# Performance work log

Hardware: AMD Instinct MI355X
Metric: run time of the kernel (lower is better)

Reference implementation:

```python
import jax, jax.numpy as jnp
import numpy as np


def _expand_chunk(x):
    # prepend the previous bucket along the chunk axis: [b, nb, bl, ...] -> [b, nb, 2*bl, ...]
    return jnp.concatenate([jnp.roll(x, 1, axis=1), x], axis=2)


def _gather_seq(origin, idx):
    # origin [b, s, d], idx [b, s, r] -> out[b, s, :, r] = origin[b, idx[b, s, r], :]
    b = origin.shape[0]
    g = origin[jnp.arange(b)[:, None, None], idx]  # [b, s, r, d]
    return jnp.transpose(g, (0, 1, 3, 2))          # [b, s, d, r]


def _count_dup_keys(inp, rounds):
    # inp [b, s, K] int32: count duplicate key indices within a window of `rounds` in sorted order
    sort_idx = jnp.argsort(inp, axis=2)
    sorted_k = jnp.take_along_axis(inp, sort_idx, axis=2)
    unsort = jnp.argsort(sort_idx, axis=2)
    cnt = jnp.ones(inp.shape, jnp.float32)
    for i in range(1, rounds):
        eq = (sorted_k[..., i:] == sorted_k[..., :-i]).astype(jnp.float32)
        pad = jnp.zeros(inp.shape[:-1] + (i,), jnp.float32)
        cnt = cnt + jnp.concatenate([pad, eq], axis=-1) + jnp.concatenate([eq, pad], axis=-1)
    return jnp.take_along_axis(cnt, unsort, axis=2)


def setup_inputs() -> dict:
    key = jax.random.key(0)
    k1, k2, k3 = jax.random.split(key, 3)
    B_M_H, SEQ, D_K, N_ROUNDS, N_BUCKETS = 32, 2048, 64, 4, 32
    query = jax.random.normal(k1, (B_M_H, SEQ, D_K), jnp.float32)
    value = jax.random.normal(k2, (B_M_H, SEQ, D_K), jnp.float32)
    rand_matrix = jax.random.normal(k3, (B_M_H, D_K, N_ROUNDS, N_BUCKETS // 2), jnp.float32)
    return {"query": query, "value": value, "rand_matrix": rand_matrix}


def reference(query, value, rand_matrix):
    b, s, d = query.shape
    nr = rand_matrix.shape[2]
    n_buckets = 2 * rand_matrix.shape[3]
    bl = s // n_buckets  # bucket_len

    # --- LSH hashing: argmax over [proj, -proj], then make hashes unique per position ---
    proj = jnp.einsum('bsd,bdrk->bsrk', query, rand_matrix)
    hashes = jnp.argmax(jnp.concatenate([proj, -proj], axis=-1), axis=-1).astype(jnp.int32)
    hashes = hashes * s + jnp.arange(s, dtype=jnp.int32)[None, :, None]  # [b, s, nr]

    sort_idx = jnp.argsort(hashes, axis=1)      # [b, s, nr]
    unsort_idx = jnp.argsort(sort_idx, axis=1)  # [b, s, nr]

    # --- sort queries into buckets ---
    q = _gather_seq(query, sort_idx).reshape(b, n_buckets, bl, d, nr)
    k = _expand_chunk(q)  # [b, nb, 2*bl, d, nr]
    k = k * jax.lax.rsqrt(jnp.maximum(jnp.sum(k * k, axis=-2, keepdims=True), 1e-12))

    qk = jnp.einsum('bnidr,bnjdr->bnijr', q, k) / np.float32(np.sqrt(d))  # [b, nb, bl, 2bl, nr]

    # --- causal / self masks on original positions ---
    qi = sort_idx.reshape(b, n_buckets, bl, nr) % s
    ki = _expand_chunk(qi)  # [b, nb, 2bl, nr]
    mask1 = (qi[:, :, :, None, :] < ki[:, :, None, :, :]).astype(jnp.float32)
    mask2 = (qi[:, :, :, None, :] == ki[:, :, None, :, :]).astype(jnp.float32)
    qk = qk * (1 - mask1) + mask1 * (-1e9)
    qk = qk * (1 - mask2) + mask2 * (-1e5)

    # --- duplicate-key counting across rounds ---
    ki_b = jnp.broadcast_to(ki[:, :, None, :, :], (b, n_buckets, bl, 2 * bl, nr)).reshape(b, s, 2 * bl * nr)
    count_keys = _count_dup_keys(ki_b, nr).reshape(b, s, 2 * bl, nr)

    qk = qk.reshape(b, s, 2 * bl, nr)
    lse = jax.scipy.special.logsumexp(qk, axis=2)  # [b, s, nr]
    sm = jnp.exp(qk - lse[:, :, None, :]) / count_keys

    v = _gather_seq(value, sort_idx).reshape(b, n_buckets, bl, d, nr)
    vk = _expand_chunk(v)  # [b, nb, 2bl, d, nr]
    sm = sm.reshape(b, n_buckets, bl, 2 * bl, nr)
    att = jnp.einsum('bnijr,bnjdr->bnidr', sm, vk).reshape(b, s, d, nr)

    # --- unsort back to original order, per round ---
    att = jnp.transpose(att, (0, 1, 3, 2))  # [b, s, nr, d]
    att = jnp.take_along_axis(att, jnp.broadcast_to(unsort_idx[:, :, :, None], att.shape), axis=1)
    lse = jnp.take_along_axis(lse, unsort_idx, axis=1)

    # --- combine rounds weighted by softmax of logsumexp ---
    w = jax.nn.softmax(lse, axis=-1)  # [b, s, nr]
    return jnp.einsum('bsrd,bsr->bsd', att, w)
```

## Files before the change

### kernel.cpp

```cpp
#include <hip/hip_runtime.h>

typedef unsigned short u16;
typedef unsigned int   u32;
typedef short bf16x8 __attribute__((ext_vector_type(8)));
typedef float f32x16 __attribute__((ext_vector_type(16)));

#define S_  2048
#define D_  64
#define NR_ 4
#define NB_ 32

#define AS 72
#define VS 136
#define PS 136

__device__ __forceinline__ float bf2f(u16 u){ return __uint_as_float(((u32)u)<<16); }
__device__ __forceinline__ u16 f2bf(float f){
  u32 u = __float_as_uint(f);
  u32 r = (u + 0x7fffu + ((u>>16)&1u)) >> 16;
  return (u16)r;
}
__device__ __forceinline__ u32 pk2bf(float a, float b){
#if __has_builtin(__builtin_amdgcn_cvt_pk_bf16_f32)
  auto r = __builtin_amdgcn_cvt_pk_bf16_f32(a, b);
  u32 u; __builtin_memcpy(&u, &r, 4); return u;
#else
  return (u32)f2bf(a) | ((u32)f2bf(b) << 16);
#endif
}
__device__ __forceinline__ u16 f2bf1(float a){ return (u16)pk2bf(a, a); }
__device__ __forceinline__ void unpack2(u32 w, float &a, float &b){
  a = __uint_as_float(w<<16);
  b = __uint_as_float(w & 0xffff0000u);
}
__device__ __forceinline__ bf16x8 ld8(const u16* p){
  union { uint4 u; bf16x8 v; } x;
  x.u = *(const uint4*)p;
  return x.v;
}

__global__ __launch_bounds__(256, 2) void k_hash(const float* __restrict__ q,
                                                 const float* __restrict__ v,
                                                 const float* __restrict__ R,
                                                 int* __restrict__ hout,
                                                 u16* __restrict__ qb,
                                                 u16* __restrict__ vbuf,
                                                 float* __restrict__ scq){
  __shared__ float Rl[4096];
  int b   = blockIdx.x >> 3;
  int pos = (blockIdx.x & 7) * 256 + threadIdx.x;

  {
    const float4* Rg = (const float4*)(R + (size_t)b * 4096);
    float4* Rs = (float4*)Rl;
    #pragma unroll
    for (int k = 0; k < 4; k++) Rs[k*256 + threadIdx.x] = Rg[k*256 + threadIdx.x];
  }
  __syncthreads();

  const float4* q4 = (const float4*)(q + ((size_t)b * S_ + pos) * D_);
  const float4* v4 = (const float4*)(v + ((size_t)b * S_ + pos) * D_);
  uint2* qw = (uint2*)(qb   + ((size_t)b * S_ + pos) * D_);
  uint2* vw = (uint2*)(vbuf + ((size_t)b * S_ + pos) * D_);

  float acc[64];
  #pragma unroll
  for (int i = 0; i < 64; i++) acc[i] = 0.f;
  float ss = 0.f;

  #pragma unroll 4
  for (int c = 0; c < 16; c++){
    float4 wa = q4[c];
    float4 xa = v4[c];
    ss += wa.x*wa.x + wa.y*wa.y + wa.z*wa.z + wa.w*wa.w;
    qw[c] = make_uint2(pk2bf(wa.x, wa.y), pk2bf(wa.z, wa.w));
    vw[c] = make_uint2(pk2bf(xa.x, xa.y), pk2bf(xa.z, xa.w));
    float qa[4] = {wa.x, wa.y, wa.z, wa.w};
    #pragma unroll
    for (int dd = 0; dd < 4; dd++){
      int d = c * 4 + dd;
      const float4* Rr = (const float4*)(&Rl[d * 64]);
      #pragma unroll
      for (int k4 = 0; k4 < 16; k4++){
        float4 rv = Rr[k4];
        acc[k4*4+0] += qa[dd] * rv.x;
        acc[k4*4+1] += qa[dd] * rv.y;
        acc[k4*4+2] += qa[dd] * rv.z;
        acc[k4*4+3] += qa[dd] * rv.w;
      }
    }
  }
  scq[(size_t)b * S_ + pos] = rsqrtf(fmaxf(ss, 1e-12f)) * 0.125f;

  #pragma unroll
  for (int r = 0; r < 4; r++){
    float bv = acc[r*16]; int bi = 0;
    #pragma unroll
    for (int m = 1; m < 32; m++){
      float vv = (m < 16) ? acc[r*16 + m] : -acc[r*16 + m - 16];
      if (vv > bv){ bv = vv; bi = m; }
    }
    hout[((size_t)b * NR_ + r) * S_ + pos] = bi;
  }
}

__global__ __launch_bounds__(256) void k_sort(const int* __restrict__ h,
                                              int* __restrict__ sidx,
                                              int* __restrict__ chk){
  __shared__ int cnt[32][257];
  __shared__ int base[32];
  int br = blockIdx.x;
  const int* hb = h + (size_t)br * S_;
  int t = threadIdx.x;

  #pragma unroll
  for (int hh = 0; hh < 32; hh++) cnt[hh][t] = 0;
  __syncthreads();

  int hv[8];
  const int4* hb4 = (const int4*)hb;
  int4 a0 = hb4[t*2], a1 = hb4[t*2+1];
  hv[0]=a0.x; hv[1]=a0.y; hv[2]=a0.z; hv[3]=a0.w;
  hv[4]=a1.x; hv[5]=a1.y; hv[6]=a1.z; hv[7]=a1.w;
  #pragma unroll
  for (int k = 0; k < 8; k++) cnt[hv[k]][t]++;
  __syncthreads();

  int wave = t >> 6, lane = t & 63;
  for (int hh = wave*8; hh < wave*8 + 8; hh++){
    int vals[4]; int s0 = 0;
    #pragma unroll
    for (int k = 0; k < 4; k++){ vals[k] = cnt[hh][lane*4+k]; s0 += vals[k]; }
    int incl = s0;
    #pragma unroll
    for (int off = 1; off < 64; off <<= 1){
      int o = __shfl_up(incl, off, 64);
      if (lane >= off) incl += o;
    }
    int run = incl - s0;
    #pragma unroll
    for (int k = 0; k < 4; k++){ int tmp = vals[k]; cnt[hh][lane*4+k] = run; run += tmp; }
    if (lane == 63) base[hh] = incl;
  }
  __syncthreads();
  if (t == 0){
    int run = 0;
    #pragma unroll
    for (int hh = 0; hh < 32; hh++){ int tot = base[hh]; base[hh] = run; run += tot; }
  }
  __syncthreads();

  int p0 = t * 8;
  #pragma unroll
  for (int k = 0; k < 8; k++){
    int hh = hv[k];
    int c = cnt[hh][t];
    int slot = base[hh] + c;
    cnt[hh][t] = c + 1;
    sidx[(size_t)br * S_ + slot]    = p0 + k;
    chk [(size_t)br * S_ + p0 + k]  = slot >> 6;
  }
}

__global__ __launch_bounds__(256, 4) void k_attn(const u16* __restrict__ qb,
                                                 const u16* __restrict__ vb,
                                                 const int* __restrict__ sidx,
                                                 const int* __restrict__ chk,
                                                 const float* __restrict__ scq,
                                                 float* __restrict__ lse_ws,
                                                 u16*  __restrict__ att_ws){
  __shared__ u16 A[128*AS];
  __shared__ u16 SM[64*PS];
  __shared__ int   pkey[128];
  __shared__ float rcnt[128];
  __shared__ float sc[128];

  int blk = blockIdx.x;
  int b = blk >> 7, r = (blk >> 5) & 3, n = blk & 31;
  int npv = (n + 31) & 31;
  int t = threadIdx.x;
  int lane = t & 63, w = t >> 6;
  int la = lane & 31, hh = lane >> 5;
  int coff = hh * 8;
  const int* sb = sidx + ((size_t)b * NR_ + r) * S_;

  if (t < 128){
    int p = (t < 64) ? sb[npv*64 + t] : sb[n*64 + (t - 64)];
    pkey[t] = p;
    int c = 0;
    #pragma unroll
    for (int rr = 0; rr < 4; rr++){
      int ch = chk[((size_t)b * NR_ + rr) * S_ + p];
      c += (ch == n) || (ch == npv);
    }
    if (c < 1) c = 1;
    rcnt[t] = 1.0f / (float)c;
    sc[t] = scq[(size_t)b * S_ + p];
  }
  __syncthreads();

  {
    int row = t >> 1, half = t & 1;
    const uint4* src = (const uint4*)(qb + ((size_t)b*S_ + pkey[row])*D_) + half*4;
    uint4* dst = (uint4*)(&A[row*AS + half*32]);
    #pragma unroll
    for (int k = 0; k < 4; k++) dst[k] = src[k];
  }
  int jp = t & 63, dgrp = t >> 6;
  uint4 va0, va1, vb0, vb1;
  {
    const uint4* s0 = (const uint4*)(vb + ((size_t)b*S_ + pkey[2*jp  ])*D_ + dgrp*16);
    const uint4* s1 = (const uint4*)(vb + ((size_t)b*S_ + pkey[2*jp+1])*D_ + dgrp*16);
    va0 = s0[0]; va1 = s0[1]; vb0 = s1[0]; vb1 = s1[1];
  }
  __syncthreads();

  {
    int jt = w;
    f32x16 acc0, acc1;
    #pragma unroll
    for (int i = 0; i < 16; i++){ acc0[i] = 0.f; acc1[i] = 0.f; }
    int arow  = (jt*32 + la) * AS;
    int brow0 = (64 + la) * AS;
    int brow1 = (96 + la) * AS;
    #pragma unroll
    for (int ks = 0; ks < 4; ks++){
      int o = ks*16 + coff;
      bf16x8 af = ld8(&A[arow  + o]);
      bf16x8 b0 = ld8(&A[brow0 + o]);
      bf16x8 b1 = ld8(&A[brow1 + o]);
      acc0 = __builtin_amdgcn_mfma_f32_32x32x16_bf16(af, b0, acc0, 0, 0, 0);
      acc1 = __builtin_amdgcn_mfma_f32_32x32x16_bf16(af, b1, acc1, 0, 0, 0);
    }
    int pj[16]; float scj[16];
    #pragma unroll
    for (int g = 0; g < 4; g++){
      int j0 = jt*32 + g*8 + 4*hh;
      #pragma unroll
      for (int m = 0; m < 4; m++){ pj[g*4+m] = pkey[j0+m]; scj[g*4+m] = sc[j0+m]; }
    }
    #pragma unroll
    for (int e = 0; e < 2; e++){
      int i = e*32 + la;
      int pi = pkey[64 + i];
      #pragma unroll
      for (int g = 0; g < 4; g++){
        float l[4];
        #pragma unroll
        for (int m = 0; m < 4; m++){
          int reg = g*4 + m;
          float x = (e ? acc1[reg] : acc0[reg]) * scj[reg];
          if (pi < pj[reg])       x = -1000000000.0f;
          else if (pi == pj[reg]) x = -100000.0f;
          l[m] = x;
        }
        int j0 = jt*32 + g*8 + 4*hh;
        *(uint2*)(&SM[i*PS + j0]) = make_uint2(pk2bf(l[0], l[1]), pk2bf(l[2], l[3]));
      }
    }
  }
  __syncthreads();

  {
    int srow = t >> 2, seg = t & 3;
    uint4 u[4];
    const uint4* p4 = (const uint4*)(&SM[srow*PS + seg*32]);
    #pragma unroll
    for (int k = 0; k < 4; k++) u[k] = p4[k];
    float vals[32];
    #pragma unroll
    for (int k = 0; k < 4; k++){
      unpack2(u[k].x, vals[k*8+0], vals[k*8+1]);
      unpack2(u[k].y, vals[k*8+2], vals[k*8+3]);
      unpack2(u[k].z, vals[k*8+4], vals[k*8+5]);
      unpack2(u[k].w, vals[k*8+6], vals[k*8+7]);
    }
    float mx = -3.0e38f;
    #pragma unroll
    for (int k = 0; k < 32; k++) mx = fmaxf(mx, vals[k]);
    float sl = 0.f;
    #pragma unroll
    for (int k = 0; k < 32; k++){ vals[k] = __expf(vals[k] - mx); sl += vals[k]; }
    float mxg = fmaxf(mx, __shfl_xor(mx, 1, 64));
    mxg = fmaxf(mxg, __shfl_xor(mxg, 2, 64));
    float scale = __expf(mx - mxg);
    float s = sl * scale;
    s += __shfl_xor(s, 1, 64);
    s += __shfl_xor(s, 2, 64);
    float f = scale / s;
    const float4* rc4 = (const float4*)(&rcnt[seg*32]);
    u32 ob[16];
    #pragma unroll
    for (int k4 = 0; k4 < 8; k4++){
      float4 rc = rc4[k4];
      ob[k4*2+0] = pk2bf(vals[k4*4+0]*f*rc.x, vals[k4*4+1]*f*rc.y);
      ob[k4*2+1] = pk2bf(vals[k4*4+2]*f*rc.z, vals[k4*4+3]*f*rc.w);
    }
    uint4* d4 = (uint4*)(&SM[srow*PS + seg*32]);
    #pragma unroll
    for (int k = 0; k < 4; k++)
      d4[k] = make_uint4(ob[4*k], ob[4*k+1], ob[4*k+2], ob[4*k+3]);
    if (seg == 0)
      lse_ws[((size_t)b*S_ + pkey[64 + srow])*NR_ + r] = mxg + __logf(s);
  }

  {
    u32 au[8] = {va0.x, va0.y, va0.z, va0.w, va1.x, va1.y, va1.z, va1.w};
    u32 bu[8] = {vb0.x, vb0.y, vb0.z, vb0.w, vb1.x, vb1.y, vb1.z, vb1.w};
    u32* vtp = (u32*)A;
    #pragma unroll
    for (int k = 0; k < 8; k++){
      int d0 = dgrp*16 + 2*k;
      u32 even = (au[k] & 0xffffu) | (bu[k] << 16);
      u32 odd  = (au[k] >> 16)     | (bu[k] & 0xffff0000u);
      vtp[ d0      * (VS/2) + jp] = even;
      vtp[(d0 + 1) * (VS/2) + jp] = odd;
    }
  }
  __syncthreads();

  {
    int Mt2 = w >> 1, Nt2 = w & 1;
    f32x16 acc;
    #pragma unroll
    for (int i = 0; i < 16; i++) acc[i] = 0.f;
    int arow = (Mt2*32 + la) * VS;
    int brow = (Nt2*32 + la) * PS;
    #pragma unroll
    for (int ks = 0; ks < 8; ks++){
      int o = ks*16 + coff;
      bf16x8 af = ld8(&A[arow + o]);
      bf16x8 bf = ld8(&SM[brow + o]);
      acc = __builtin_amdgcn_mfma_f32_32x32x16_bf16(af, bf, acc, 0, 0, 0);
    }
    int i = Nt2*32 + la;
    int p = pkey[64 + i];
    u16* base = att_ws + (((size_t)b*S_ + p)*NR_ + r)*D_ + Mt2*32 + 4*hh;
    #pragma unroll
    for (int g = 0; g < 4; g++){
      uint2 val = make_uint2(pk2bf(acc[4*g+0], acc[4*g+1]),
                             pk2bf(acc[4*g+2], acc[4*g+3]));
      *(uint2*)(base + g*8) = val;
    }
  }
}

__global__ __launch_bounds__(256) void k_comb(const float* __restrict__ lse_ws,
                                              const u16* __restrict__ att_ws,
                                              float* __restrict__ out){
  size_t idx4 = (size_t)blockIdx.x * 256 + threadIdx.x;
  size_t pd = idx4 >> 4;
  int d0 = (int)(idx4 & 15) * 4;
  float4 lv = *(const float4*)(lse_ws + pd * 4);
  float m = fmaxf(fmaxf(lv.x, lv.y), fmaxf(lv.z, lv.w));
  float e0 = __expf(lv.x - m), e1 = __expf(lv.y - m);
  float e2 = __expf(lv.z - m), e3 = __expf(lv.w - m);
  float inv = 1.0f / (e0 + e1 + e2 + e3);
  e0 *= inv; e1 *= inv; e2 *= inv; e3 *= inv;
  const u16* a = att_ws + pd * 256 + d0;
  uint2 u0 = *(const uint2*)(a);
  uint2 u1 = *(const uint2*)(a + 64);
  uint2 u2 = *(const uint2*)(a + 128);
  uint2 u3 = *(const uint2*)(a + 192);
  float4 o;
  float a0,b0,a1,b1,a2,b2,a3,b3;
  unpack2(u0.x,a0,b0); unpack2(u1.x,a1,b1); unpack2(u2.x,a2,b2); unpack2(u3.x,a3,b3);
  o.x = a0*e0 + a1*e1 + a2*e2 + a3*e3;
  o.y = b0*e0 + b1*e1 + b2*e2 + b3*e3;
  unpack2(u0.y,a0,b0); unpack2(u1.y,a1,b1); unpack2(u2.y,a2,b2); unpack2(u3.y,a3,b3);
  o.z = a0*e0 + a1*e1 + a2*e2 + a3*e3;
  o.w = b0*e0 + b1*e1 + b2*e2 + b3*e3;
  *(float4*)(out + pd * D_ + d0) = o;
}

extern "C" void kernel_launch(void* const* d_in, const int* in_sizes, int n_in,
                              void* d_out, int out_size, void* d_ws, size_t ws_size,
                              hipStream_t stream){
  const float* q = (const float*)d_in[0];
  const float* v = (const float*)d_in[1];
  const float* R = (const float*)d_in[2];

  char* w = (char*)d_ws;
  int*   h    = (int*)  (w + 0);
  int*   sidx = (int*)  (w + (size_t)(1u << 20));
  int*   chkA = (int*)  (w + (size_t)(2u << 20));
  float* lse  = (float*)(w + (size_t)(3u << 20));
  u16*   att  = (u16*)  (w + (size_t)(4u << 20));
  u16*   qb   = (u16*)  (w + (size_t)(36u << 20));
  u16*   vbuf = (u16*)  (w + (size_t)(44u << 20));
  float* scq  = (float*)(w + (size_t)(52u << 20));
  float* out  = (float*)d_out;

  k_hash <<<256,  256, 0, stream>>>(q, v, R, h, qb, vbuf, scq);
  k_sort <<<128,  256, 0, stream>>>(h, sidx, chkA);
  k_attn <<<4096, 256, 0, stream>>>(qb, vbuf, sidx, chkA, scq, lse, att);
  k_comb <<<4096, 256, 0, stream>>>(lse, att, out);
}
```

Before: 150.7 us.

## Compute softmax in MFMA registers with cross-wave partial max/sum reduction

Softmax over the QK logits now runs directly on the MFMA accumulator registers. Each wave computes per-row partial max and sum, combines the two half-waves with shuffles, and exchanges partials across waves through small shared arrays. This removes the bf16 round trip of raw logits through shared memory and the separate re-read pass, and keeps logits in fp32 until the final probabilities are written. In exchange it holds more live registers, so the occupancy hint in launch bounds drops from 4 to 3 blocks.

```diff
diff --git a/kernel.cpp b/kernel.cpp
--- a/kernel.cpp
+++ b/kernel.cpp
@@ -162,7 +162,7 @@
   }
 }
 
-__global__ __launch_bounds__(256, 4) void k_attn(const u16* __restrict__ qb,
+__global__ __launch_bounds__(256, 3) void k_attn(const u16* __restrict__ qb,
                                                  const u16* __restrict__ vb,
                                                  const int* __restrict__ sidx,
                                                  const int* __restrict__ chk,
@@ -174,6 +174,8 @@
   __shared__ int   pkey[128];
   __shared__ float rcnt[128];
   __shared__ float sc[128];
+  __shared__ float pm[4*64];
+  __shared__ float ps[4*64];
 
   int blk = blockIdx.x;
   int b = blk >> 7, r = (blk >> 5) & 3, n = blk & 31;
@@ -215,6 +217,8 @@
   }
   __syncthreads();
 
+  float e0[16], e1[16];
+  float ml0, ml1;
   {
     int jt = w;
     f32x16 acc0, acc1;
@@ -239,71 +243,70 @@
       #pragma unroll
       for (int m = 0; m < 4; m++){ pj[g*4+m] = pkey[j0+m]; scj[g*4+m] = sc[j0+m]; }
     }
-    #pragma unroll
-    for (int e = 0; e < 2; e++){
-      int i = e*32 + la;
-      int pi = pkey[64 + i];
-      #pragma unroll
-      for (int g = 0; g < 4; g++){
-        float l[4];
-        #pragma unroll
-        for (int m = 0; m < 4; m++){
-          int reg = g*4 + m;
-          float x = (e ? acc1[reg] : acc0[reg]) * scj[reg];
-          if (pi < pj[reg])       x = -1000000000.0f;
-          else if (pi == pj[reg]) x = -100000.0f;
-          l[m] = x;
-        }
-        int j0 = jt*32 + g*8 + 4*hh;
-        *(uint2*)(&SM[i*PS + j0]) = make_uint2(pk2bf(l[0], l[1]), pk2bf(l[2], l[3]));
-      }
-    }
-  }
-  __syncthreads();
-
-  {
-    int srow = t >> 2, seg = t & 3;
-    uint4 u[4];
-    const uint4* p4 = (const uint4*)(&SM[srow*PS + seg*32]);
-    #pragma unroll
-    for (int k = 0; k < 4; k++) u[k] = p4[k];
-    float vals[32];
+    int pi0 = pkey[64 + la], pi1 = pkey[96 + la];
+    float x0[16], x1[16];
+    #pragma unroll
+    for (int reg = 0; reg < 16; reg++){
+      float a0v = acc0[reg] * scj[reg];
+      float a1v = acc1[reg] * scj[reg];
+      if (pi0 < pj[reg]) a0v = -1000000000.0f; else if (pi0 == pj[reg]) a0v = -100000.0f;
+      if (pi1 < pj[reg]) a1v = -1000000000.0f; else if (pi1 == pj[reg]) a1v = -100000.0f;
+      x0[reg] = a0v; x1[reg] = a1v;
+    }
+    ml0 = x0[0]; ml1 = x1[0];
+    #pragma unroll
+    for (int reg = 1; reg < 16; reg++){ ml0 = fmaxf(ml0, x0[reg]); ml1 = fmaxf(ml1, x1[reg]); }
+    float s0 = 0.f, s1 = 0.f;
+    #pragma unroll
+    for (int reg = 0; reg < 16; reg++){
+      e0[reg] = __expf(x0[reg] - ml0); s0 += e0[reg];
+      e1[reg] = __expf(x1[reg] - ml1); s1 += e1[reg];
+    }
+    float om0 = __shfl_xor(ml0, 32, 64), os0 = __shfl_xor(s0, 32, 64);
+    float om1 = __shfl_xor(ml1, 32, 64), os1 = __shfl_xor(s1, 32, 64);
+    float m20 = fmaxf(ml0, om0);
+    float m21 = fmaxf(ml1, om1);
+    float s20 = s0 * __expf(ml0 - m20) + os0 * __expf(om0 - m20);
+    float s21 = s1 * __expf(ml1 - m21) + os1 * __expf(om1 - m21);
+    if (hh == 0){
+      pm[jt*64 + la]      = m20;  ps[jt*64 + la]      = s20;
+      pm[jt*64 + 32 + la] = m21;  ps[jt*64 + 32 + la] = s21;
+    }
+  }
+  __syncthreads();
+
+  {
+    int jt = w;
+    float mg0 = pm[la],      mg1 = pm[32 + la];
+    #pragma unroll
+    for (int k = 1; k < 4; k++){
+      mg0 = fmaxf(mg0, pm[k*64 + la]);
+      mg1 = fmaxf(mg1, pm[k*64 + 32 + la]);
+    }
+    float sg0 = 0.f, sg1 = 0.f;
     #pragma unroll
     for (int k = 0; k < 4; k++){
-      unpack2(u[k].x, vals[k*8+0], vals[k*8+1]);
-      unpack2(u[k].y, vals[k*8+2], vals[k*8+3]);
-      unpack2(u[k].z, vals[k*8+4], vals[k*8+5]);
-      unpack2(u[k].w, vals[k*8+6], vals[k*8+7]);
-    }
-    float mx = -3.0e38f;
-    #pragma unroll
-    for (int k = 0; k < 32; k++) mx = fmaxf(mx, vals[k]);
-    float sl = 0.f;
-    #pragma unroll
-    for (int k = 0; k < 32; k++){ vals[k] = __expf(vals[k] - mx); sl += vals[k]; }
-    float mxg = fmaxf(mx, __shfl_xor(mx, 1, 64));
-    mxg = fmaxf(mxg, __shfl_xor(mxg, 2, 64));
-    float scale = __expf(mx - mxg);
-    float s = sl * scale;
-    s += __shfl_xor(s, 1, 64);
-    s += __shfl_xor(s, 2, 64);
-    float f = scale / s;
-    const float4* rc4 = (const float4*)(&rcnt[seg*32]);
-    u32 ob[16];
-    #pragma unroll
-    for (int k4 = 0; k4 < 8; k4++){
-      float4 rc = rc4[k4];
-      ob[k4*2+0] = pk2bf(vals[k4*4+0]*f*rc.x, vals[k4*4+1]*f*rc.y);
-      ob[k4*2+1] = pk2bf(vals[k4*4+2]*f*rc.z, vals[k4*4+3]*f*rc.w);
-    }
-    uint4* d4 = (uint4*)(&SM[srow*PS + seg*32]);
-    #pragma unroll
-    for (int k = 0; k < 4; k++)
-      d4[k] = make_uint4(ob[4*k], ob[4*k+1], ob[4*k+2], ob[4*k+3]);
-    if (seg == 0)
-      lse_ws[((size_t)b*S_ + pkey[64 + srow])*NR_ + r] = mxg + __logf(s);
-  }
-
+      sg0 += ps[k*64 + la]      * __expf(pm[k*64 + la]      - mg0);
+      sg1 += ps[k*64 + 32 + la] * __expf(pm[k*64 + 32 + la] - mg1);
+    }
+    float f0 = __expf(ml0 - mg0) / sg0;
+    float f1 = __expf(ml1 - mg1) / sg1;
+    #pragma unroll
+    for (int g = 0; g < 4; g++){
+      int j0 = jt*32 + g*8 + 4*hh;
+      float4 rc = *(const float4*)(&rcnt[j0]);
+      float p00 = e0[g*4+0]*f0*rc.x, p01 = e0[g*4+1]*f0*rc.y;
+      float p02 = e0[g*4+2]*f0*rc.z, p03 = e0[g*4+3]*f0*rc.w;
+      float p10 = e1[g*4+0]*f1*rc.x, p11 = e1[g*4+1]*f1*rc.y;
+      float p12 = e1[g*4+2]*f1*rc.z, p13 = e1[g*4+3]*f1*rc.w;
+      *(uint2*)(&SM[la*PS + j0])        = make_uint2(pk2bf(p00,p01), pk2bf(p02,p03));
+      *(uint2*)(&SM[(32+la)*PS + j0])   = make_uint2(pk2bf(p10,p11), pk2bf(p12,p13));
+    }
+    if (w == 0 && hh == 0){
+      lse_ws[((size_t)b*S_ + pkey[64 + la])*NR_ + r] = mg0 + __logf(sg0);
+      lse_ws[((size_t)b*S_ + pkey[96 + la])*NR_ + r] = mg1 + __logf(sg1);
+    }
+  }
   {
     u32 au[8] = {va0.x, va0.y, va0.z, va0.w, va1.x, va1.y, va1.z, va1.w};
     u32 bu[8] = {vb0.x, vb0.y, vb0.z, vb0.w, vb1.x, vb1.y, vb1.z, vb1.w};
```

Result: no change. 149.0 us (median of 3 runs) (-1.1%).
